# Optimization experiments

Hardware: AMD Instinct MI355X
Metric: run time of the kernel (lower is better)

The kernel has to match this reference:

```python
import jax, jax.numpy as jnp
import numpy as np


def setup_inputs() -> dict:
    key = jax.random.key(0)
    k1, k2, k3 = jax.random.split(key, 3)
    B, D, L = 16384, 1024, 4
    x = jax.random.normal(k1, (B, D), dtype=jnp.float32)
    weights = jax.random.normal(k2, (L, D, 1), dtype=jnp.float32)
    biases = jax.random.normal(k3, (L, D, 1), dtype=jnp.float32)
    return {"x": x, "weights": weights, "biases": biases}


def reference(x, weights, biases):
    # DCN cross layer. Literal torch math per layer:
    #   out = (x[:,:,None] @ out[:,None,:] @ w_i + b_i).squeeze(-1) + out
    # Algebraically identical (associativity of matmul):
    #   out = x * (out @ w_i) + b_i.T + out
    w = weights[..., 0]  # (L, D)
    b = biases[..., 0]   # (L, D)

    def step(out, wb):
        w_i, b_i = wb
        s = out @ w_i  # (B,) scalar per row: out . w_i
        out = x * s[:, None] + b_i[None, :] + out
        return out, None

    out, _ = jax.lax.scan(step, x, (w, b))
    return out
```

## Files before the change

### kernel.cpp

```cpp
#include <hip/hip_runtime.h>


typedef float v4f __attribute__((ext_vector_type(4)));

constexpr int D  = 1024;
constexpr int D4 = D / 4;
constexpr int L  = 4;
constexpr int WAVES_PER_BLOCK = 4;
constexpr int ROWS_PER_WAVE   = 8;
constexpr int CHUNK           = 2;
constexpr int NCH             = ROWS_PER_WAVE / CHUNK;
constexpr int ROWS_PER_BLOCK  = WAVES_PER_BLOCK * ROWS_PER_WAVE;

template<int CTRL>
__device__ __forceinline__ float dpp_add(float v) {
    int t = __builtin_amdgcn_update_dpp(0, __float_as_int(v), CTRL, 0xF, 0xF, true);
    return v + __int_as_float(t);
}

__device__ __forceinline__ float wave_sum(float v) {
    v = dpp_add<0x111>(v);
    v = dpp_add<0x112>(v);
    v = dpp_add<0x114>(v);
    v = dpp_add<0x118>(v);
    v = dpp_add<0x142>(v);
    v = dpp_add<0x143>(v);
    return __int_as_float(__builtin_amdgcn_readlane(__float_as_int(v), 63));
}

__device__ __forceinline__ float hsum(v4f a) { return (a.x + a.y) + (a.z + a.w); }

__global__ __launch_bounds__(256) void cross_layer_kernel(
    const float* __restrict__ x,
    const float* __restrict__ w,
    const float* __restrict__ b,
    float* __restrict__ out,
    int B)
{
    const int tid  = threadIdx.x;
    const int lane = tid & 63;
    const int wave = tid >> 6;
    const int row0 = blockIdx.x * ROWS_PER_BLOCK + wave * ROWS_PER_WAVE;

    const v4f* w4 = reinterpret_cast<const v4f*>(w);
    const v4f* b4 = reinterpret_cast<const v4f*>(b);
    const v4f* x4 = reinterpret_cast<const v4f*>(x);

    v4f wr[L][4];
    #pragma unroll
    for (int l = 0; l < L; ++l)
        #pragma unroll
        for (int c = 0; c < 4; ++c)
            wr[l][c] = w4[l * D4 + lane + c * 64];

    v4f bt[L][4];
    #pragma unroll
    for (int l = 0; l < L; ++l)
        #pragma unroll
        for (int c = 0; c < 4; ++c)
            bt[l][c] = b4[l * D4 + lane + c * 64];

    v4f xb[NCH][CHUNK][4];
    #pragma unroll
    for (int r = 0; r < CHUNK; ++r) {
        const int row = row0 + r;
        if (row < B) {
            #pragma unroll
            for (int c = 0; c < 4; ++c)
                xb[0][r][c] = __builtin_nontemporal_load(&x4[(size_t)row * D4 + lane + c * 64]);
        } else {
            #pragma unroll
            for (int c = 0; c < 4; ++c) xb[0][r][c] = (v4f)(0.f);
        }
    }

    v4f p[4] = {(v4f)(0.f), (v4f)(0.f), (v4f)(0.f), (v4f)(0.f)};
    float epart[3];
    #pragma unroll
    for (int l = 0; l < L; ++l) {
        if (l >= 1) {
            v4f ea = p[0] * wr[l][0];
            #pragma unroll
            for (int c = 1; c < 4; ++c) ea += p[c] * wr[l][c];
            epart[l - 1] = hsum(ea);
        }
        #pragma unroll
        for (int c = 0; c < 4; ++c) p[c] += bt[l][c];
    }
    float e1 = wave_sum(epart[0]);
    float e2 = wave_sum(epart[1]);
    float e3 = wave_sum(epart[2]);

    #pragma unroll
    for (int r = 0; r < CHUNK; ++r) {
        const int row = row0 + CHUNK + r;
        if (row < B) {
            #pragma unroll
            for (int c = 0; c < 4; ++c)
                xb[1][r][c] = __builtin_nontemporal_load(&x4[(size_t)row * D4 + lane + c * 64]);
        } else {
            #pragma unroll
            for (int c = 0; c < 4; ++c) xb[1][r][c] = (v4f)(0.f);
        }
    }

    #pragma unroll
    for (int k = 0; k < NCH; ++k) {
        if (k + 2 < NCH) {
            #pragma unroll
            for (int r = 0; r < CHUNK; ++r) {
                const int row = row0 + (k + 2) * CHUNK + r;
                if (row < B) {
                    #pragma unroll
                    for (int c = 0; c < 4; ++c)
                        xb[k + 2][r][c] = __builtin_nontemporal_load(&x4[(size_t)row * D4 + lane + c * 64]);
                } else {
                    #pragma unroll
                    for (int c = 0; c < 4; ++c) xb[k + 2][r][c] = (v4f)(0.f);
                }
            }
        }

        float dd[CHUNK][L];
        #pragma unroll
        for (int r = 0; r < CHUNK; ++r) {
            #pragma unroll
            for (int l = 0; l < L; ++l) {
                v4f a = xb[k][r][0] * wr[l][0];
                #pragma unroll
                for (int c = 1; c < 4; ++c)
                    a += xb[k][r][c] * wr[l][c];
                dd[r][l] = hsum(a);
            }
        }
        #pragma unroll
        for (int r = 0; r < CHUNK; ++r)
            #pragma unroll
            for (int l = 0; l < L; ++l)
                dd[r][l] = wave_sum(dd[r][l]);

        #pragma unroll
        for (int r = 0; r < CHUNK; ++r) {
            const int row = row0 + k * CHUNK + r;
            if (row < B) {
                float a = 1.f + dd[r][0];
                a = a + a * dd[r][1] + e1;
                a = a + a * dd[r][2] + e2;
                a = a + a * dd[r][3] + e3;
                v4f* o4 = reinterpret_cast<v4f*>(out) + (size_t)row * D4;
                #pragma unroll
                for (int c = 0; c < 4; ++c) {
                    v4f v = xb[k][r][c] * a + p[c];
                    __builtin_nontemporal_store(v, &o4[lane + c * 64]);
                }
            }
        }
    }
}

extern "C" void kernel_launch(void* const* d_in, const int* in_sizes, int n_in,
                              void* d_out, int out_size, void* d_ws, size_t ws_size,
                              hipStream_t stream) {
    const float* x  = (const float*)d_in[0];
    const float* w  = (const float*)d_in[1];
    const float* b  = (const float*)d_in[2];
    float* out      = (float*)d_out;

    const int B = in_sizes[0] / D;
    const int blocks = (B + ROWS_PER_BLOCK - 1) / ROWS_PER_BLOCK;
    cross_layer_kernel<<<blocks, 256, 0, stream>>>(x, w, b, out, B);
}
```

Measured before the change: 121.9 us.

## Halve rows per wave, load all rows upfront, use regular loads/stores

Reduces rows per wave from 8 to 4, which doubles the block count. It replaces the rolling two-chunk prefetch pipeline with a single upfront load of all x rows. Nontemporal loads and stores become ordinary ones. The aim is more parallelism and simpler issue of memory operations. In exchange, each block reloads the weights and biases twice as often, and the cache behaviour of the streaming traffic may change.

After: 119.3 us. 2.1% less time.

```diff
diff --git a/kernel.cpp b/kernel.cpp
--- a/kernel.cpp
+++ b/kernel.cpp
@@ -7,7 +7,7 @@
 constexpr int D4 = D / 4;
 constexpr int L  = 4;
 constexpr int WAVES_PER_BLOCK = 4;
-constexpr int ROWS_PER_WAVE   = 8;
+constexpr int ROWS_PER_WAVE   = 4;
 constexpr int CHUNK           = 2;
 constexpr int NCH             = ROWS_PER_WAVE / CHUNK;
 constexpr int ROWS_PER_BLOCK  = WAVES_PER_BLOCK * ROWS_PER_WAVE;
@@ -62,15 +62,18 @@
 
     v4f xb[NCH][CHUNK][4];
     #pragma unroll
-    for (int r = 0; r < CHUNK; ++r) {
-        const int row = row0 + r;
-        if (row < B) {
-            #pragma unroll
-            for (int c = 0; c < 4; ++c)
-                xb[0][r][c] = __builtin_nontemporal_load(&x4[(size_t)row * D4 + lane + c * 64]);
-        } else {
-            #pragma unroll
-            for (int c = 0; c < 4; ++c) xb[0][r][c] = (v4f)(0.f);
+    for (int k = 0; k < NCH; ++k) {
+        #pragma unroll
+        for (int r = 0; r < CHUNK; ++r) {
+            const int row = row0 + k * CHUNK + r;
+            if (row < B) {
+                #pragma unroll
+                for (int c = 0; c < 4; ++c)
+                    xb[k][r][c] = x4[(size_t)row * D4 + lane + c * 64];
+            } else {
+                #pragma unroll
+                for (int c = 0; c < 4; ++c) xb[k][r][c] = (v4f)(0.f);
+            }
         }
     }
 
@@ -87,40 +90,12 @@
         #pragma unroll
         for (int c = 0; c < 4; ++c) p[c] += bt[l][c];
     }
-    float e1 = wave_sum(epart[0]);
-    float e2 = wave_sum(epart[1]);
-    float e3 = wave_sum(epart[2]);
-
-    #pragma unroll
-    for (int r = 0; r < CHUNK; ++r) {
-        const int row = row0 + CHUNK + r;
-        if (row < B) {
-            #pragma unroll
-            for (int c = 0; c < 4; ++c)
-                xb[1][r][c] = __builtin_nontemporal_load(&x4[(size_t)row * D4 + lane + c * 64]);
-        } else {
-            #pragma unroll
-            for (int c = 0; c < 4; ++c) xb[1][r][c] = (v4f)(0.f);
-        }
-    }
+    const float e1 = wave_sum(epart[0]);
+    const float e2 = wave_sum(epart[1]);
+    const float e3 = wave_sum(epart[2]);
 
     #pragma unroll
     for (int k = 0; k < NCH; ++k) {
-        if (k + 2 < NCH) {
-            #pragma unroll
-            for (int r = 0; r < CHUNK; ++r) {
-                const int row = row0 + (k + 2) * CHUNK + r;
-                if (row < B) {
-                    #pragma unroll
-                    for (int c = 0; c < 4; ++c)
-                        xb[k + 2][r][c] = __builtin_nontemporal_load(&x4[(size_t)row * D4 + lane + c * 64]);
-                } else {
-                    #pragma unroll
-                    for (int c = 0; c < 4; ++c) xb[k + 2][r][c] = (v4f)(0.f);
-                }
-            }
-        }
-
         float dd[CHUNK][L];
         #pragma unroll
         for (int r = 0; r < CHUNK; ++r) {
@@ -149,10 +124,8 @@
                 a = a + a * dd[r][3] + e3;
                 v4f* o4 = reinterpret_cast<v4f*>(out) + (size_t)row * D4;
                 #pragma unroll
-                for (int c = 0; c < 4; ++c) {
-                    v4f v = xb[k][r][c] * a + p[c];
-                    __builtin_nontemporal_store(v, &o4[lane + c * 64]);
-                }
+                for (int c = 0; c < 4; ++c)
+                    o4[lane + c * 64] = xb[k][r][c] * a + p[c];
             }
         }
     }
```
